# Kernel tuning notes

Measured on AMD Instinct MI355X. Metric: run time of the kernel, lower is better.

The kernel has to match this reference:

```python
import jax, jax.numpy as jnp
import numpy as np

B, T, D = 4, 256, 256
H, DK = 4, 64
NUM_REL = 64
EPS = 1e-5


def setup_inputs() -> dict:
    key = jax.random.key(0)
    ks = jax.random.split(key, 16)
    s = 0.02
    return {
        "node_features": jax.random.normal(ks[0], (B, T, D), jnp.float32),
        "spatial_matrix": jax.random.randint(ks[1], (B, T, T), 0, NUM_REL, jnp.int32),
        "Wq": jax.random.normal(ks[2], (D, D), jnp.float32) * s,
        "bq": jnp.zeros((D,), jnp.float32),
        "Wk": jax.random.normal(ks[3], (D, D), jnp.float32) * s,
        "bk": jnp.zeros((D,), jnp.float32),
        "Wv": jax.random.normal(ks[4], (D, D), jnp.float32) * s,
        "bv": jnp.zeros((D,), jnp.float32),
        "rel_k": jax.random.normal(ks[5], (NUM_REL, D), jnp.float32) * s,
        "rel_v": jax.random.normal(ks[6], (NUM_REL, D), jnp.float32) * s,
        "Wo": jax.random.normal(ks[7], (D, D), jnp.float32) * s,
        "bo": jnp.zeros((D,), jnp.float32),
        "gamma": jnp.ones((D,), jnp.float32),
        "beta": jnp.zeros((D,), jnp.float32),
    }


def reference(node_features, spatial_matrix, Wq, bq, Wk, bk, Wv, bv,
              rel_k, rel_v, Wo, bo, gamma, beta):
    b, t, d = node_features.shape
    # projections -> [B,T,H,dk]
    q = (node_features @ Wq.T + bq).reshape(b, t, H, DK)
    k = (node_features @ Wk.T + bk).reshape(b, t, H, DK)
    v = (node_features @ Wv.T + bv).reshape(b, t, H, DK)
    # per-edge relation embeddings -> [B,T,T,H,dk]
    r_k = rel_k[spatial_matrix].reshape(b, t, t, H, DK)
    r_v = rel_v[spatial_matrix].reshape(b, t, t, H, DK)
    # k' = k_j + r_{ij}; scores[b,i,j,h] = <q_i, k'_{ij}> / sqrt(dk)
    k_prime = k[:, None, :, :, :] + r_k
    scores = jnp.einsum('bihd,bijhd->bijh', q, k_prime) / jnp.sqrt(jnp.float32(DK))
    attn = jax.nn.softmax(scores, axis=2)  # over key index j (dropout p used in eval => identity)
    v_prime = v[:, None, :, :, :] + r_v
    agg = jnp.einsum('bijh,bijhd->bihd', attn, v_prime).reshape(b, t, d)
    out = agg @ Wo.T + bo + node_features
    # LayerNorm over last dim
    mu = jnp.mean(out, axis=-1, keepdims=True)
    var = jnp.var(out, axis=-1, keepdims=True)
    out = (out - mu) / jnp.sqrt(var + EPS) * gamma + beta
    return jax.nn.relu(out)
```

## Files before the change

kernel.cpp:

```cpp
#include <hip/hip_runtime.h>

#define TT 256
#define DD 256
#define NH 4
#define DKK 64
#define NR 64
#define NB 4

__global__ __launch_bounds__(256) void k_qkv(
    const float* __restrict__ x,
    const float* __restrict__ Wq, const float* __restrict__ bq,
    const float* __restrict__ Wk, const float* __restrict__ bk,
    const float* __restrict__ Wv, const float* __restrict__ bv,
    float* __restrict__ Q, float* __restrict__ K, float* __restrict__ V)
{
    const int z = blockIdx.z;
    const float* __restrict__ W    = (z == 0) ? Wq : (z == 1) ? Wk : Wv;
    const float* __restrict__ bias = (z == 0) ? bq : (z == 1) ? bk : bv;
    float* __restrict__ out        = (z == 0) ? Q  : (z == 1) ? K  : V;
    const int r0 = blockIdx.x * 16, c0 = blockIdx.y * 64;
    __shared__ float xl[16][68];
    __shared__ float wl[64][68];
    const int t = threadIdx.x;
    const int cg = t & 15, rg = t >> 4;
    float acc[4] = {};
    for (int kt = 0; kt < 4; ++kt) {
        const int kb = kt * 64;
        {
            const int r = t >> 4, q4 = t & 15;
            *(float4*)&xl[r][q4 * 4] = *(const float4*)&x[(r0 + r) * DD + kb + q4 * 4];
        }
        #pragma unroll
        for (int u = 0; u < 4; ++u) {
            const int idx = u * 256 + t;
            const int r = idx >> 4, q4 = idx & 15;
            *(float4*)&wl[r][q4 * 4] = *(const float4*)&W[(c0 + r) * DD + kb + q4 * 4];
        }
        __syncthreads();
        #pragma unroll 4
        for (int d4 = 0; d4 < 64; d4 += 4) {
            const float4 xv = *(const float4*)&xl[rg][d4];
            #pragma unroll
            for (int c = 0; c < 4; ++c) {
                const float4 wv = *(const float4*)&wl[cg + 16 * c][d4];
                acc[c] += xv.x * wv.x + xv.y * wv.y + xv.z * wv.z + xv.w * wv.w;
            }
        }
        __syncthreads();
    }
    const int r = r0 + rg;
    #pragma unroll
    for (int c = 0; c < 4; ++c) {
        const int cc = c0 + cg + 16 * c;
        out[r * DD + cc] = acc[c] + bias[cc];
    }
}

__global__ __launch_bounds__(512) void k_attn(
    const float* __restrict__ Q, const float* __restrict__ K, const float* __restrict__ V,
    const int* __restrict__ SM,
    const float* __restrict__ relk, const float* __restrict__ relv,
    float* __restrict__ AGG)
{
    const int it = blockIdx.x, h = blockIdx.y, b = blockIdx.z;
    const int i0 = it * 16;
    __shared__ float kv[256][68];
    __shared__ float ql[16][68];
    __shared__ float rkl[64][68];
    __shared__ float rvl[64][68];
    __shared__ float sl[16][260];
    __shared__ float qrl[16][64];
    __shared__ float wlh[16][64];
    __shared__ union { int sml[16][256]; float aggp[4][16][64]; } uu;

    const int t = threadIdx.x;

    if (t < 256) {
        const int r = t >> 4, q4 = t & 15;
        *(float4*)&ql[r][q4 * 4] = *(const float4*)&Q[(b * TT + i0 + r) * DD + h * DKK + q4 * 4];
    }
    #pragma unroll
    for (int u = 0; u < 2; ++u) {
        const int idx = u * 512 + t;
        const int r = idx >> 4, q4 = idx & 15;
        *(float4*)&rkl[r][q4 * 4] = *(const float4*)&relk[r * DD + h * DKK + q4 * 4];
        *(float4*)&rvl[r][q4 * 4] = *(const float4*)&relv[r * DD + h * DKK + q4 * 4];
    }
    #pragma unroll
    for (int u = 0; u < 2; ++u) {
        const int idx = u * 512 + t;
        const int i = idx >> 6, j4 = idx & 63;
        *(int4*)&uu.sml[i][j4 * 4] = *(const int4*)&SM[(b * TT + i0 + i) * TT + j4 * 4];
    }
    #pragma unroll
    for (int u = 0; u < 8; ++u) {
        const int idx = u * 512 + t;
        const int j = idx >> 4, q4 = idx & 15;
        *(float4*)&kv[j][q4 * 4] = *(const float4*)&K[(b * TT + j) * DD + h * DKK + q4 * 4];
    }
    __syncthreads();

    {
        const int r = t & 63, ig = t >> 6;
        float a0 = 0.f, a1 = 0.f;
        #pragma unroll 4
        for (int d4 = 0; d4 < 64; d4 += 4) {
            const float4 rk4 = *(const float4*)&rkl[r][d4];
            const float4 q0 = *(const float4*)&ql[ig * 2 + 0][d4];
            const float4 q1 = *(const float4*)&ql[ig * 2 + 1][d4];
            a0 += q0.x * rk4.x + q0.y * rk4.y + q0.z * rk4.z + q0.w * rk4.w;
            a1 += q1.x * rk4.x + q1.y * rk4.y + q1.z * rk4.z + q1.w * rk4.w;
        }
        qrl[ig * 2 + 0][r] = a0;
        qrl[ig * 2 + 1][r] = a1;
    }
    __syncthreads();

    {
        const int j = t & 255, ih = t >> 8;
        float4 kr[16];
        #pragma unroll
        for (int c = 0; c < 16; ++c) kr[c] = *(const float4*)&kv[j][c * 4];
        #pragma unroll
        for (int ii = 0; ii < 8; ++ii) {
            const int i = ih * 8 + ii;
            float a = 0.f;
            #pragma unroll
            for (int c = 0; c < 16; ++c) {
                const float4 q4 = *(const float4*)&ql[i][c * 4];
                a += q4.x * kr[c].x + q4.y * kr[c].y + q4.z * kr[c].z + q4.w * kr[c].w;
            }
            sl[i][j] = (a + qrl[i][uu.sml[i][j]]) * 0.125f;
        }
    }
    {
        float* wf = &wlh[0][0];
        wf[t] = 0.f; wf[t + 512] = 0.f;
    }

    float4 vpre[8];
    #pragma unroll
    for (int u = 0; u < 8; ++u) {
        const int idx = u * 512 + t;
        const int j = idx >> 4, q4 = idx & 15;
        vpre[u] = *(const float4*)&V[(b * TT + j) * DD + h * DKK + q4 * 4];
    }
    __syncthreads();

    {
        const int row = t >> 5, g = t & 31;
        float vals[8];
        float m = -1e30f;
        #pragma unroll
        for (int jj = 0; jj < 8; ++jj) {
            vals[jj] = sl[row][g + jj * 32];
            m = fmaxf(m, vals[jj]);
        }
        #pragma unroll
        for (int off = 16; off; off >>= 1) m = fmaxf(m, __shfl_xor(m, off, 32));
        float s = 0.f;
        #pragma unroll
        for (int jj = 0; jj < 8; ++jj) { vals[jj] = __expf(vals[jj] - m); s += vals[jj]; }
        #pragma unroll
        for (int off = 16; off; off >>= 1) s += __shfl_xor(s, off, 32);
        const float inv = 1.0f / s;
        #pragma unroll
        for (int jj = 0; jj < 8; ++jj) {
            const float p = vals[jj] * inv;
            sl[row][g + jj * 32] = p;
            atomicAdd(&wlh[row][uu.sml[row][g + jj * 32]], p);
        }
    }
    __syncthreads();

    #pragma unroll
    for (int u = 0; u < 8; ++u) {
        const int idx = u * 512 + t;
        const int j = idx >> 4, q4 = idx & 15;
        *(float4*)&kv[j][q4 * 4] = vpre[u];
    }
    __syncthreads();

    {
        const int w = t >> 6, l = t & 63;
        const int jq = w >> 1, ih = w & 1;
        const int dg = l & 15, ig = l >> 4;
        const int ia = ih * 8 + ig * 2;
        float4 ac0 = {0,0,0,0}, ac1 = {0,0,0,0};
        const int jb = jq * 64;
        for (int j0 = jb; j0 < jb + 64; j0 += 4) {
            const float4 p0 = *(const float4*)&sl[ia + 0][j0];
            const float4 p1 = *(const float4*)&sl[ia + 1][j0];
            float4 v4;
            v4 = *(const float4*)&kv[j0 + 0][dg * 4];
            ac0.x += p0.x*v4.x; ac0.y += p0.x*v4.y; ac0.z += p0.x*v4.z; ac0.w += p0.x*v4.w;
            ac1.x += p1.x*v4.x; ac1.y += p1.x*v4.y; ac1.z += p1.x*v4.z; ac1.w += p1.x*v4.w;
            v4 = *(const float4*)&kv[j0 + 1][dg * 4];
            ac0.x += p0.y*v4.x; ac0.y += p0.y*v4.y; ac0.z += p0.y*v4.z; ac0.w += p0.y*v4.w;
            ac1.x += p1.y*v4.x; ac1.y += p1.y*v4.y; ac1.z += p1.y*v4.z; ac1.w += p1.y*v4.w;
            v4 = *(const float4*)&kv[j0 + 2][dg * 4];
            ac0.x += p0.z*v4.x; ac0.y += p0.z*v4.y; ac0.z += p0.z*v4.z; ac0.w += p0.z*v4.w;
            ac1.x += p1.z*v4.x; ac1.y += p1.z*v4.y; ac1.z += p1.z*v4.z; ac1.w += p1.z*v4.w;
            v4 = *(const float4*)&kv[j0 + 3][dg * 4];
            ac0.x += p0.w*v4.x; ac0.y += p0.w*v4.y; ac0.z += p0.w*v4.z; ac0.w += p0.w*v4.w;
            ac1.x += p1.w*v4.x; ac1.y += p1.w*v4.y; ac1.z += p1.w*v4.z; ac1.w += p1.w*v4.w;
        }
        *(float4*)&uu.aggp[jq][ia + 0][dg * 4] = ac0;
        *(float4*)&uu.aggp[jq][ia + 1][dg * 4] = ac1;
    }
    __syncthreads();

    {
        const int d = t & 63, w = t >> 6;
        const int ia = w * 2;
        float a0 = uu.aggp[0][ia+0][d] + uu.aggp[1][ia+0][d] + uu.aggp[2][ia+0][d] + uu.aggp[3][ia+0][d];
        float a1 = uu.aggp[0][ia+1][d] + uu.aggp[1][ia+1][d] + uu.aggp[2][ia+1][d] + uu.aggp[3][ia+1][d];
        for (int r = 0; r < 64; ++r) {
            const float rv = rvl[r][d];
            a0 += wlh[ia + 0][r] * rv;
            a1 += wlh[ia + 1][r] * rv;
        }
        AGG[(b * TT + i0 + ia + 0) * DD + h * DKK + d] = a0;
        AGG[(b * TT + i0 + ia + 1) * DD + h * DKK + d] = a1;
    }
}

__global__ __launch_bounds__(256) void k_oproj(
    const float* __restrict__ AGG, const float* __restrict__ Wo,
    const float* __restrict__ bo, const float* __restrict__ x,
    float* __restrict__ OPRE)
{
    const int r0 = blockIdx.x * 16, c0 = blockIdx.y * 64;
    __shared__ float al[16][68];
    __shared__ float wl[64][68];
    const int t = threadIdx.x;
    const int cg = t & 15, rg = t >> 4;
    float acc[4] = {};
    for (int kt = 0; kt < 4; ++kt) {
        const int kb = kt * 64;
        {
            const int r = t >> 4, q4 = t & 15;
            *(float4*)&al[r][q4 * 4] = *(const float4*)&AGG[(r0 + r) * DD + kb + q4 * 4];
        }
        #pragma unroll
        for (int u = 0; u < 4; ++u) {
            const int idx = u * 256 + t;
            const int r = idx >> 4, q4 = idx & 15;
            *(float4*)&wl[r][q4 * 4] = *(const float4*)&Wo[(c0 + r) * DD + kb + q4 * 4];
        }
        __syncthreads();
        #pragma unroll 4
        for (int d4 = 0; d4 < 64; d4 += 4) {
            const float4 av = *(const float4*)&al[rg][d4];
            #pragma unroll
            for (int c = 0; c < 4; ++c) {
                const float4 wv = *(const float4*)&wl[cg + 16 * c][d4];
                acc[c] += av.x * wv.x + av.y * wv.y + av.z * wv.z + av.w * wv.w;
            }
        }
        __syncthreads();
    }
    const int r = r0 + rg;
    #pragma unroll
    for (int c = 0; c < 4; ++c) {
        const int cc = c0 + cg + 16 * c;
        OPRE[r * DD + cc] = acc[c] + bo[cc] + x[r * DD + cc];
    }
}

__global__ __launch_bounds__(256) void k_ln(
    const float* __restrict__ OPRE, const float* __restrict__ gamma,
    const float* __restrict__ beta, float* __restrict__ out)
{
    const int row = blockIdx.x * 4 + (threadIdx.x >> 6);
    const int lane = threadIdx.x & 63;
    const float4 v = *(const float4*)&OPRE[row * DD + lane * 4];
    float s  = v.x + v.y + v.z + v.w;
    float sq = v.x * v.x + v.y * v.y + v.z * v.z + v.w * v.w;
    #pragma unroll
    for (int off = 32; off; off >>= 1) {
        s  += __shfl_xor(s, off, 64);
        sq += __shfl_xor(sq, off, 64);
    }
    const float mu   = s * (1.0f / DD);
    const float rstd = rsqrtf(sq * (1.0f / DD) - mu * mu + 1e-5f);
    const float4 g  = *(const float4*)&gamma[lane * 4];
    const float4 bt = *(const float4*)&beta[lane * 4];
    float4 o;
    o.x = fmaxf((v.x - mu) * rstd * g.x + bt.x, 0.f);
    o.y = fmaxf((v.y - mu) * rstd * g.y + bt.y, 0.f);
    o.z = fmaxf((v.z - mu) * rstd * g.z + bt.z, 0.f);
    o.w = fmaxf((v.w - mu) * rstd * g.w + bt.w, 0.f);
    *(float4*)&out[row * DD + lane * 4] = o;
}

extern "C" void kernel_launch(void* const* d_in, const int* in_sizes, int n_in,
                              void* d_out, int out_size, void* d_ws, size_t ws_size,
                              hipStream_t stream)
{
    (void)in_sizes; (void)n_in; (void)out_size; (void)ws_size;
    const float* x     = (const float*)d_in[0];
    const int*   SM    = (const int*)d_in[1];
    const float* Wq    = (const float*)d_in[2];
    const float* bq    = (const float*)d_in[3];
    const float* Wk    = (const float*)d_in[4];
    const float* bk    = (const float*)d_in[5];
    const float* Wv    = (const float*)d_in[6];
    const float* bv    = (const float*)d_in[7];
    const float* relk  = (const float*)d_in[8];
    const float* relv  = (const float*)d_in[9];
    const float* Wo    = (const float*)d_in[10];
    const float* bo    = (const float*)d_in[11];
    const float* gamma = (const float*)d_in[12];
    const float* beta  = (const float*)d_in[13];
    float* out = (float*)d_out;
    float* ws  = (float*)d_ws;

    const int NTD = NB * TT * DD;
    float* Q  = ws;
    float* K  = ws + NTD;
    float* V  = ws + 2 * NTD;
    float* AG = ws + 3 * NTD;
    float* OP = ws + 4 * NTD;

    k_qkv  <<<dim3(64, 4, 3), 256, 0, stream>>>(x, Wq, bq, Wk, bk, Wv, bv, Q, K, V);
    k_attn <<<dim3(16, NH, NB), 512, 0, stream>>>(Q, K, V, SM, relk, relv, AG);
    k_oproj<<<dim3(64, 4), 256, 0, stream>>>(AG, Wo, bo, x, OP);
    k_ln   <<<256, 256, 0, stream>>>(OP, gamma, beta, out);
}
```

Measured before the change: 128.4 us.

## Slim attention kernel: 256 threads, direct global K/V/rel reads, byte-packed relation indices

The attention kernel drops the 68KB shared-memory K/V staging buffer and the rel_k/rel_v tiles. K, V and the relation tables are now read straight from global memory (through cache) into registers, and the relation indices are packed into bytes in shared memory. Block size is halved to 256 threads, and each thread handles more rows, which cuts the shared-memory footprint and should let more blocks sit on each CU. The price is repeated global/L2 reads of V and rel_v in place of LDS reuse, and fewer threads per block.

Measured after the change: 135.3 us. +5.4%, slower.

```diff
diff --git a/kernel.cpp b/kernel.cpp
--- a/kernel.cpp
+++ b/kernel.cpp
@@ -6,6 +6,8 @@
 #define DKK 64
 #define NR 64
 #define NB 4
+
+#define FMA4(A, S, V) { A.x += (S)*(V).x; A.y += (S)*(V).y; A.z += (S)*(V).z; A.w += (S)*(V).w; }
 
 __global__ __launch_bounds__(256) void k_qkv(
     const float* __restrict__ x,
@@ -56,7 +58,7 @@
     }
 }
 
-__global__ __launch_bounds__(512) void k_attn(
+__global__ __launch_bounds__(256) void k_attn(
     const float* __restrict__ Q, const float* __restrict__ K, const float* __restrict__ V,
     const int* __restrict__ SM,
     const float* __restrict__ relk, const float* __restrict__ relv,
@@ -64,164 +66,150 @@
 {
     const int it = blockIdx.x, h = blockIdx.y, b = blockIdx.z;
     const int i0 = it * 16;
-    __shared__ float kv[256][68];
     __shared__ float ql[16][68];
-    __shared__ float rkl[64][68];
-    __shared__ float rvl[64][68];
+    __shared__ unsigned char smlp[16][256];
     __shared__ float sl[16][260];
     __shared__ float qrl[16][64];
     __shared__ float wlh[16][64];
-    __shared__ union { int sml[16][256]; float aggp[4][16][64]; } uu;
+    __shared__ float aggp[4][16][68];
 
     const int t = threadIdx.x;
 
-    if (t < 256) {
+    {
         const int r = t >> 4, q4 = t & 15;
         *(float4*)&ql[r][q4 * 4] = *(const float4*)&Q[(b * TT + i0 + r) * DD + h * DKK + q4 * 4];
     }
     #pragma unroll
-    for (int u = 0; u < 2; ++u) {
-        const int idx = u * 512 + t;
-        const int r = idx >> 4, q4 = idx & 15;
-        *(float4*)&rkl[r][q4 * 4] = *(const float4*)&relk[r * DD + h * DKK + q4 * 4];
-        *(float4*)&rvl[r][q4 * 4] = *(const float4*)&relv[r * DD + h * DKK + q4 * 4];
-    }
-    #pragma unroll
-    for (int u = 0; u < 2; ++u) {
-        const int idx = u * 512 + t;
+    for (int u = 0; u < 4; ++u) {
+        const int idx = u * 256 + t;
         const int i = idx >> 6, j4 = idx & 63;
-        *(int4*)&uu.sml[i][j4 * 4] = *(const int4*)&SM[(b * TT + i0 + i) * TT + j4 * 4];
-    }
-    #pragma unroll
-    for (int u = 0; u < 8; ++u) {
-        const int idx = u * 512 + t;
-        const int j = idx >> 4, q4 = idx & 15;
-        *(float4*)&kv[j][q4 * 4] = *(const float4*)&K[(b * TT + j) * DD + h * DKK + q4 * 4];
+        const int4 s4 = *(const int4*)&SM[(b * TT + i0 + i) * TT + j4 * 4];
+        const unsigned int pk = (unsigned int)(s4.x & 255) | ((unsigned int)(s4.y & 255) << 8)
+                              | ((unsigned int)(s4.z & 255) << 16) | ((unsigned int)(s4.w & 255) << 24);
+        *(unsigned int*)&smlp[i][j4 * 4] = pk;
+    }
+    {
+        float* wf = &wlh[0][0];
+        wf[t] = 0.f; wf[t + 256] = 0.f; wf[t + 512] = 0.f; wf[t + 768] = 0.f;
     }
     __syncthreads();
 
     {
         const int r = t & 63, ig = t >> 6;
-        float a0 = 0.f, a1 = 0.f;
+        const float* __restrict__ rk = &relk[r * DD + h * DKK];
+        float a0 = 0.f, a1 = 0.f, a2 = 0.f, a3 = 0.f;
         #pragma unroll 4
         for (int d4 = 0; d4 < 64; d4 += 4) {
-            const float4 rk4 = *(const float4*)&rkl[r][d4];
-            const float4 q0 = *(const float4*)&ql[ig * 2 + 0][d4];
-            const float4 q1 = *(const float4*)&ql[ig * 2 + 1][d4];
+            const float4 rk4 = *(const float4*)&rk[d4];
+            const float4 q0 = *(const float4*)&ql[ig * 4 + 0][d4];
+            const float4 q1 = *(const float4*)&ql[ig * 4 + 1][d4];
+            const float4 q2 = *(const float4*)&ql[ig * 4 + 2][d4];
+            const float4 q3 = *(const float4*)&ql[ig * 4 + 3][d4];
             a0 += q0.x * rk4.x + q0.y * rk4.y + q0.z * rk4.z + q0.w * rk4.w;
             a1 += q1.x * rk4.x + q1.y * rk4.y + q1.z * rk4.z + q1.w * rk4.w;
-        }
-        qrl[ig * 2 + 0][r] = a0;
-        qrl[ig * 2 + 1][r] = a1;
-    }
-    __syncthreads();
-
-    {
-        const int j = t & 255, ih = t >> 8;
+            a2 += q2.x * rk4.x + q2.y * rk4.y + q2.z * rk4.z + q2.w * rk4.w;
+            a3 += q3.x * rk4.x + q3.y * rk4.y + q3.z * rk4.z + q3.w * rk4.w;
+        }
+        qrl[ig * 4 + 0][r] = a0;
+        qrl[ig * 4 + 1][r] = a1;
+        qrl[ig * 4 + 2][r] = a2;
+        qrl[ig * 4 + 3][r] = a3;
+    }
+    __syncthreads();
+
+    {
+        const int j = t;
+        const float* __restrict__ kro = &K[(b * TT + j) * DD + h * DKK];
         float4 kr[16];
         #pragma unroll
-        for (int c = 0; c < 16; ++c) kr[c] = *(const float4*)&kv[j][c * 4];
-        #pragma unroll
-        for (int ii = 0; ii < 8; ++ii) {
-            const int i = ih * 8 + ii;
+        for (int c = 0; c < 16; ++c) kr[c] = *(const float4*)&kro[c * 4];
+        for (int i = 0; i < 16; ++i) {
             float a = 0.f;
             #pragma unroll
             for (int c = 0; c < 16; ++c) {
                 const float4 q4 = *(const float4*)&ql[i][c * 4];
                 a += q4.x * kr[c].x + q4.y * kr[c].y + q4.z * kr[c].z + q4.w * kr[c].w;
             }
-            sl[i][j] = (a + qrl[i][uu.sml[i][j]]) * 0.125f;
-        }
-    }
-    {
-        float* wf = &wlh[0][0];
-        wf[t] = 0.f; wf[t + 512] = 0.f;
-    }
-
-    float4 vpre[8];
-    #pragma unroll
-    for (int u = 0; u < 8; ++u) {
-        const int idx = u * 512 + t;
-        const int j = idx >> 4, q4 = idx & 15;
-        vpre[u] = *(const float4*)&V[(b * TT + j) * DD + h * DKK + q4 * 4];
-    }
-    __syncthreads();
-
-    {
-        const int row = t >> 5, g = t & 31;
-        float vals[8];
+            sl[i][j] = (a + qrl[i][smlp[i][j]]) * 0.125f;
+        }
+    }
+    __syncthreads();
+
+    {
+        const int row = t >> 4, g = t & 15;
+        float vals[16];
         float m = -1e30f;
         #pragma unroll
-        for (int jj = 0; jj < 8; ++jj) {
-            vals[jj] = sl[row][g + jj * 32];
+        for (int jj = 0; jj < 16; ++jj) {
+            vals[jj] = sl[row][g + jj * 16];
             m = fmaxf(m, vals[jj]);
         }
         #pragma unroll
-        for (int off = 16; off; off >>= 1) m = fmaxf(m, __shfl_xor(m, off, 32));
+        for (int off = 8; off; off >>= 1) m = fmaxf(m, __shfl_xor(m, off, 16));
         float s = 0.f;
         #pragma unroll
-        for (int jj = 0; jj < 8; ++jj) { vals[jj] = __expf(vals[jj] - m); s += vals[jj]; }
-        #pragma unroll
-        for (int off = 16; off; off >>= 1) s += __shfl_xor(s, off, 32);
+        for (int jj = 0; jj < 16; ++jj) { vals[jj] = __expf(vals[jj] - m); s += vals[jj]; }
+        #pragma unroll
+        for (int off = 8; off; off >>= 1) s += __shfl_xor(s, off, 16);
         const float inv = 1.0f / s;
         #pragma unroll
-        for (int jj = 0; jj < 8; ++jj) {
+        for (int jj = 0; jj < 16; ++jj) {
             const float p = vals[jj] * inv;
-            sl[row][g + jj * 32] = p;
-            atomicAdd(&wlh[row][uu.sml[row][g + jj * 32]], p);
-        }
-    }
-    __syncthreads();
-
-    #pragma unroll
-    for (int u = 0; u < 8; ++u) {
-        const int idx = u * 512 + t;
-        const int j = idx >> 4, q4 = idx & 15;
-        *(float4*)&kv[j][q4 * 4] = vpre[u];
+            sl[row][g + jj * 16] = p;
+            atomicAdd(&wlh[row][smlp[row][g + jj * 16]], p);
+        }
     }
     __syncthreads();
 
     {
         const int w = t >> 6, l = t & 63;
-        const int jq = w >> 1, ih = w & 1;
         const int dg = l & 15, ig = l >> 4;
-        const int ia = ih * 8 + ig * 2;
-        float4 ac0 = {0,0,0,0}, ac1 = {0,0,0,0};
-        const int jb = jq * 64;
-        for (int j0 = jb; j0 < jb + 64; j0 += 4) {
-            const float4 p0 = *(const float4*)&sl[ia + 0][j0];
-            const float4 p1 = *(const float4*)&sl[ia + 1][j0];
-            float4 v4;
-            v4 = *(const float4*)&kv[j0 + 0][dg * 4];
-            ac0.x += p0.x*v4.x; ac0.y += p0.x*v4.y; ac0.z += p0.x*v4.z; ac0.w += p0.x*v4.w;
-            ac1.x += p1.x*v4.x; ac1.y += p1.x*v4.y; ac1.z += p1.x*v4.z; ac1.w += p1.x*v4.w;
-            v4 = *(const float4*)&kv[j0 + 1][dg * 4];
-            ac0.x += p0.y*v4.x; ac0.y += p0.y*v4.y; ac0.z += p0.y*v4.z; ac0.w += p0.y*v4.w;
-            ac1.x += p1.y*v4.x; ac1.y += p1.y*v4.y; ac1.z += p1.y*v4.z; ac1.w += p1.y*v4.w;
-            v4 = *(const float4*)&kv[j0 + 2][dg * 4];
-            ac0.x += p0.z*v4.x; ac0.y += p0.z*v4.y; ac0.z += p0.z*v4.z; ac0.w += p0.z*v4.w;
-            ac1.x += p1.z*v4.x; ac1.y += p1.z*v4.y; ac1.z += p1.z*v4.z; ac1.w += p1.z*v4.w;
-            v4 = *(const float4*)&kv[j0 + 3][dg * 4];
-            ac0.x += p0.w*v4.x; ac0.y += p0.w*v4.y; ac0.z += p0.w*v4.z; ac0.w += p0.w*v4.w;
-            ac1.x += p1.w*v4.x; ac1.y += p1.w*v4.y; ac1.z += p1.w*v4.z; ac1.w += p1.w*v4.w;
-        }
-        *(float4*)&uu.aggp[jq][ia + 0][dg * 4] = ac0;
-        *(float4*)&uu.aggp[jq][ia + 1][dg * 4] = ac1;
-    }
-    __syncthreads();
-
-    {
-        const int d = t & 63, w = t >> 6;
-        const int ia = w * 2;
-        float a0 = uu.aggp[0][ia+0][d] + uu.aggp[1][ia+0][d] + uu.aggp[2][ia+0][d] + uu.aggp[3][ia+0][d];
-        float a1 = uu.aggp[0][ia+1][d] + uu.aggp[1][ia+1][d] + uu.aggp[2][ia+1][d] + uu.aggp[3][ia+1][d];
+        const int jb = w * 64;
+        float4 a0 = {0,0,0,0}, a1 = {0,0,0,0}, a2 = {0,0,0,0}, a3 = {0,0,0,0};
+        for (int c8 = 0; c8 < 8; ++c8) {
+            const int j0 = jb + c8 * 8;
+            float4 vr[8];
+            #pragma unroll
+            for (int u = 0; u < 8; ++u)
+                vr[u] = *(const float4*)&V[(b * TT + j0 + u) * DD + h * DKK + dg * 4];
+            #pragma unroll
+            for (int ii = 0; ii < 4; ++ii) {
+                const int i = ig * 4 + ii;
+                const float4 pa = *(const float4*)&sl[i][j0];
+                const float4 pb = *(const float4*)&sl[i][j0 + 4];
+                float4& A = (ii == 0) ? a0 : (ii == 1) ? a1 : (ii == 2) ? a2 : a3;
+                FMA4(A, pa.x, vr[0]); FMA4(A, pa.y, vr[1]);
+                FMA4(A, pa.z, vr[2]); FMA4(A, pa.w, vr[3]);
+                FMA4(A, pb.x, vr[4]); FMA4(A, pb.y, vr[5]);
+                FMA4(A, pb.z, vr[6]); FMA4(A, pb.w, vr[7]);
+            }
+        }
+        *(float4*)&aggp[w][ig * 4 + 0][dg * 4] = a0;
+        *(float4*)&aggp[w][ig * 4 + 1][dg * 4] = a1;
+        *(float4*)&aggp[w][ig * 4 + 2][dg * 4] = a2;
+        *(float4*)&aggp[w][ig * 4 + 3][dg * 4] = a3;
+    }
+    __syncthreads();
+
+    {
+        const int d = t & 63, g4 = t >> 6;
+        const int ia = g4 * 4;
+        float a0 = aggp[0][ia+0][d] + aggp[1][ia+0][d] + aggp[2][ia+0][d] + aggp[3][ia+0][d];
+        float a1 = aggp[0][ia+1][d] + aggp[1][ia+1][d] + aggp[2][ia+1][d] + aggp[3][ia+1][d];
+        float a2 = aggp[0][ia+2][d] + aggp[1][ia+2][d] + aggp[2][ia+2][d] + aggp[3][ia+2][d];
+        float a3 = aggp[0][ia+3][d] + aggp[1][ia+3][d] + aggp[2][ia+3][d] + aggp[3][ia+3][d];
+        #pragma unroll 4
         for (int r = 0; r < 64; ++r) {
-            const float rv = rvl[r][d];
+            const float rv = relv[r * DD + h * DKK + d];
             a0 += wlh[ia + 0][r] * rv;
             a1 += wlh[ia + 1][r] * rv;
+            a2 += wlh[ia + 2][r] * rv;
+            a3 += wlh[ia + 3][r] * rv;
         }
         AGG[(b * TT + i0 + ia + 0) * DD + h * DKK + d] = a0;
         AGG[(b * TT + i0 + ia + 1) * DD + h * DKK + d] = a1;
+        AGG[(b * TT + i0 + ia + 2) * DD + h * DKK + d] = a2;
+        AGG[(b * TT + i0 + ia + 3) * DD + h * DKK + d] = a3;
     }
 }
 
@@ -324,7 +312,7 @@
     float* OP = ws + 4 * NTD;
 
     k_qkv  <<<dim3(64, 4, 3), 256, 0, stream>>>(x, Wq, bq, Wk, bk, Wv, bv, Q, K, V);
-    k_attn <<<dim3(16, NH, NB), 512, 0, stream>>>(Q, K, V, SM, relk, relv, AG);
+    k_attn <<<dim3(16, NH, NB), 256, 0, stream>>>(Q, K, V, SM, relk, relv, AG);
     k_oproj<<<dim3(64, 4), 256, 0, stream>>>(AG, Wo, bo, x, OP);
     k_ln   <<<256, 256, 0, stream>>>(OP, gamma, beta, out);
 }
```
